# Optimization experiments

Hardware: AMD Instinct MI355X
Metric: run time of the kernel (lower is better)

## Reference

```python
import jax, jax.numpy as jnp
import numpy as np

B, S = 1, 128            # batch, timesteps
N_LGN = 17400            # LGN input units (dense_shape[1])
N_POST = 50000           # V1 neurons (dense_shape[0])
NNZ = 800000             # number of synapses
N_BASIS = 5              # synaptic receptor basis functions
N_RECEPT = 10            # receptor types


def setup_inputs() -> dict:
    key = jax.random.key(0)
    k1, k2, k3, k4, k5, k6 = jax.random.split(key, 6)
    inp = jax.random.normal(k1, (B, S, N_LGN), dtype=jnp.float32)
    rows = jax.random.randint(k2, (NNZ,), 0, N_POST)
    cols = jax.random.randint(k3, (NNZ,), 0, N_LGN)
    indices = jnp.stack([rows, cols], axis=1)  # [nnz, 2] sparse coords
    weights = jax.random.normal(k4, (NNZ,), dtype=jnp.float32)
    synaptic_weights = jax.random.uniform(k5, (N_RECEPT, N_BASIS), dtype=jnp.float32)
    syn_ids = jax.random.randint(k6, (NNZ,), 0, N_RECEPT)
    return {
        "inp": inp,
        "indices": indices,
        "weights": weights,
        "synaptic_weights": synaptic_weights,
        "syn_ids": syn_ids,
        "n_neurons": N_POST,
    }


def reference(inp, indices, weights, synaptic_weights, syn_ids, n_neurons):
    b, s, n_lgn = inp.shape
    x = inp.reshape(b * s, n_lgn)               # [Bt, n_lgn], Bt = batch*time
    rows = indices[:, 0]                        # post-synaptic neuron id
    cols = indices[:, 1]                        # pre-synaptic LGN id
    factors = synaptic_weights[syn_ids]         # [nnz, n_basis] (tf.gather)
    xg = x.T[cols]                              # [nnz, Bt] gathered presyn activity
    n_basis = factors.shape[1]
    outs = []
    for r in range(n_basis):                    # small fixed loop over receptor bases
        vals = weights * factors[:, r]          # per-receptor sparse values
        # sparse_dense_matmul(sparse_w_in, inp, adjoint_b=True) == scatter-add over rows
        outs.append(jax.ops.segment_sum(xg * vals[:, None], rows, num_segments=n_neurons))
    i_in = jnp.stack(outs)                      # [n_basis, n_post, Bt]
    out = jnp.transpose(i_in, (2, 1, 0))        # [Bt, n_post, n_basis]
    return out.reshape(b, s, -1)                # [batch, time, n_post*n_basis]
```

## Files before the change

### kernel.cpp

```cpp
#include <hip/hip_runtime.h>
#include <hip/hip_bf16.h>
#include <stdint.h>

#define N_LGN   17400
#define N_POST  50000
#define NNZ     800000
#define N_BASIS 5
#define ELL_CAP 48

#define NBKT      196
#define NBKT_H    391
#define CAPB      5120
#define BIN_CHUNK 4096
#define BIN_BLOCKS ((NNZ + BIN_CHUNK - 1) / BIN_CHUNK)

#define TPOSE_CBLK   32
#define TPOSE_BLOCKS ((N_LGN + TPOSE_CBLK - 1) / TPOSE_CBLK)

__global__ __launch_bounds__(256) void k_prep(const float* __restrict__ inp,
                                              __hip_bfloat162* __restrict__ xTb,
                                              const int2* __restrict__ idx2,
                                              const float* __restrict__ w,
                                              const int* __restrict__ syn,
                                              int* __restrict__ bucketCnt,
                                              int2* __restrict__ bEdges) {
    __shared__ alignas(16) int2 ebuf[BIN_CHUNK];
    __shared__ unsigned char sbuf[BIN_CHUNK];
    __shared__ int hcnt[256], hstart[256], hcur[256], gbase[256];
    int tid = threadIdx.x;
    if (blockIdx.x < BIN_BLOCKS) {
        int base = blockIdx.x * BIN_CHUNK;
        int ne = NNZ - base; if (ne > BIN_CHUNK) ne = BIN_CHUNK;
        hcnt[tid] = 0;
        __syncthreads();
        int2 pk[16]; int bk[16];
#pragma unroll
        for (int i = 0; i < 16; ++i) {
            int p = i * 256 + tid;
            bk[i] = -1;
            if (p < ne) {
                int2 rc = idx2[base + p];
                float wv = w[base + p];
                int sy = syn[base + p];
                int b  = rc.x >> 8;
                int rl = rc.x & 255;
                pk[i] = make_int2(rc.y | (sy << 15) | (rl << 19), __float_as_int(wv));
                bk[i] = b;
                atomicAdd(&hcnt[b], 1);
            }
        }
        __syncthreads();
        int v = hcnt[tid];
        hstart[tid] = v;
        __syncthreads();
        for (int off = 1; off < 256; off <<= 1) {
            int t = (tid >= off) ? hstart[tid - off] : 0;
            __syncthreads();
            hstart[tid] += t;
            __syncthreads();
        }
        int excl = hstart[tid] - v;
        hstart[tid] = excl;
        hcur[tid]  = excl;
        if (tid < NBKT) gbase[tid] = atomicAdd(&bucketCnt[tid], v);
        __syncthreads();
#pragma unroll
        for (int i = 0; i < 16; ++i) {
            if (bk[i] >= 0) {
                int pos = atomicAdd(&hcur[bk[i]], 1);
                ebuf[pos] = pk[i];
                sbuf[pos] = (unsigned char)bk[i];
            }
        }
        __syncthreads();
        for (int p = tid; p < ne; p += 256) {
            int b  = sbuf[p];
            int gi = gbase[b] + (p - hstart[b]);
            if (gi < CAPB) bEdges[b * CAPB + gi] = ebuf[p];
        }
    } else {
        float* tile = (float*)ebuf;
        int c0 = (blockIdx.x - BIN_BLOCKS) * TPOSE_CBLK;
        for (int it = 0; it < 16; ++it) {
            int flat = it * 256 + tid;
            int s  = flat >> 5;
            int cl = flat & 31;
            int c  = c0 + cl;
            float v = 0.0f;
            if (c < N_LGN) v = inp[s * N_LGN + c];
            tile[cl * 129 + s] = v;
        }
        __syncthreads();
        for (int it = 0; it < 8; ++it) {
            int flat = it * 256 + tid;
            int cl = flat >> 6;
            int sp = flat & 63;
            int c  = c0 + cl;
            if (c < N_LGN) {
                float2 f = make_float2(tile[cl * 129 + 2 * sp], tile[cl * 129 + 2 * sp + 1]);
                xTb[c * 64 + sp] = __float22bfloat162_rn(f);
            }
        }
    }
}

__global__ __launch_bounds__(512) void k_build(const int2* __restrict__ bEdges,
                                               const int* __restrict__ bucketCnt,
                                               int2* __restrict__ ell,
                                               int* __restrict__ counts) {
    __shared__ alignas(16) int2 slab[128 * ELL_CAP];
    __shared__ int rcnt[128];
    int tid   = threadIdx.x;
    int hb    = blockIdx.x;
    int B     = hb >> 1;
    int rbase = (hb & 1) << 7;
    if (tid < 128) rcnt[tid] = 0;
    {
        int4* s4w = (int4*)slab;
        for (int i = tid; i < 128 * ELL_CAP / 2; i += 512) s4w[i] = make_int4(0, 0, 0, 0);
    }
    __syncthreads();
    int cnt = bucketCnt[B]; if (cnt > CAPB) cnt = CAPB;
    for (int p = tid; p < cnt; p += 512) {
        int2 e = bEdges[B * CAPB + p];
        int rl = (e.x >> 19) & 0xFF;
        int r2 = rl - rbase;
        if ((unsigned)r2 < 128u) {
            int r = atomicAdd(&rcnt[r2], 1);
            if (r < ELL_CAP)
                slab[r2 * ELL_CAP + r] =
                    make_int2((e.x & 0x7FFF) | (((e.x >> 15) & 0xF) << 16), e.y);
        }
    }
    __syncthreads();
    int row0  = hb << 7;
    int nrows = N_POST - row0; if (nrows > 128) nrows = 128;
    if (nrows <= 0) return;
    const int4* s4 = (const int4*)slab;
    int4* e4 = (int4*)(ell + (size_t)row0 * ELL_CAP);
    int n4 = nrows * ELL_CAP / 2;
    for (int i = tid; i < n4; i += 512) e4[i] = s4[i];
    if (tid < nrows) counts[row0 + tid] = rcnt[tid];
}

__global__ __launch_bounds__(256) void k_transpose_bf16(const float* __restrict__ inp,
                                                        __hip_bfloat162* __restrict__ xTb) {
    __shared__ float tile[64 * 129];
    int c0  = blockIdx.x * 64;
    int tid = threadIdx.x;
    for (int it = 0; it < 32; ++it) {
        int flat = it * 256 + tid;
        int s  = flat >> 6;
        int cl = flat & 63;
        int c  = c0 + cl;
        float v = 0.0f;
        if (c < N_LGN) v = inp[s * N_LGN + c];
        tile[cl * 129 + s] = v;
    }
    __syncthreads();
    for (int it = 0; it < 16; ++it) {
        int flat = it * 256 + tid;
        int cl = flat >> 6;
        int sp = flat & 63;
        int c  = c0 + cl;
        if (c < N_LGN) {
            float2 f = make_float2(tile[cl * 129 + 2 * sp], tile[cl * 129 + 2 * sp + 1]);
            xTb[c * 64 + sp] = __float22bfloat162_rn(f);
        }
    }
}

__global__ __launch_bounds__(256) void k_hist(const int4* __restrict__ idx2,
                                              int* __restrict__ counts) {
    int t = blockIdx.x * 256 + threadIdx.x;
    if (t >= NNZ / 2) return;
    int4 rc = idx2[t];
    atomicAdd(&counts[rc.x], 1);
    atomicAdd(&counts[rc.z], 1);
}

__global__ __launch_bounds__(1024) void k_scan1(const int* __restrict__ counts,
                                                int* __restrict__ rowStart,
                                                int* __restrict__ blockSums) {
    __shared__ int tmp[1024];
    int tid = threadIdx.x;
    int gid = blockIdx.x * 1024 + tid;
    int v = (gid < N_POST) ? counts[gid] : 0;
    tmp[tid] = v;
    __syncthreads();
    for (int off = 1; off < 1024; off <<= 1) {
        int t = (tid >= off) ? tmp[tid - off] : 0;
        __syncthreads();
        tmp[tid] += t;
        __syncthreads();
    }
    if (gid < N_POST) rowStart[gid] = tmp[tid] - v;
    if (tid == 1023) blockSums[blockIdx.x] = tmp[1023];
}

__global__ __launch_bounds__(64) void k_scan2(const int* __restrict__ blockSums,
                                              int* __restrict__ blockOffsets, int nblk) {
    __shared__ int tmp[64];
    int tid = threadIdx.x;
    int v = (tid < nblk) ? blockSums[tid] : 0;
    tmp[tid] = v;
    __syncthreads();
    for (int off = 1; off < 64; off <<= 1) {
        int t = (tid >= off) ? tmp[tid - off] : 0;
        __syncthreads();
        tmp[tid] += t;
        __syncthreads();
    }
    if (tid < nblk) blockOffsets[tid] = tmp[tid] - v;
}

__global__ __launch_bounds__(1024) void k_scan3(int* __restrict__ rowStart,
                                                const int* __restrict__ blockOffsets) {
    int gid = blockIdx.x * 1024 + threadIdx.x;
    if (gid < N_POST) rowStart[gid] += blockOffsets[blockIdx.x];
}

__global__ __launch_bounds__(256) void k_scatter_csr(const int4* __restrict__ idx2,
                                                     const float2* __restrict__ w2,
                                                     const int2* __restrict__ syn2,
                                                     const int* __restrict__ rowStart,
                                                     int* __restrict__ cursor,
                                                     int2* __restrict__ edges) {
    int t = blockIdx.x * 256 + threadIdx.x;
    if (t >= NNZ / 2) return;
    int4 rc = idx2[t];
    float2 ww = w2[t];
    int2 sy = syn2[t];
    int p0 = rowStart[rc.x] + atomicAdd(&cursor[rc.x], 1);
    edges[p0] = make_int2(rc.y | (sy.x << 16), __float_as_int(ww.x));
    int p1 = rowStart[rc.z] + atomicAdd(&cursor[rc.z], 1);
    edges[p1] = make_int2(rc.w | (sy.y << 16), __float_as_int(ww.y));
}

#define EDGE_FMA2(P0, P1, XW, FA, F4)                                             \
    P0[0] = fmaf((XW).x, (FA).x, P0[0]); P1[0] = fmaf((XW).y, (FA).x, P1[0]);     \
    P0[1] = fmaf((XW).x, (FA).y, P0[1]); P1[1] = fmaf((XW).y, (FA).y, P1[1]);     \
    P0[2] = fmaf((XW).x, (FA).z, P0[2]); P1[2] = fmaf((XW).y, (FA).z, P1[2]);     \
    P0[3] = fmaf((XW).x, (FA).w, P0[3]); P1[3] = fmaf((XW).y, (FA).w, P1[3]);     \
    P0[4] = fmaf((XW).x, (F4),   P0[4]); P1[4] = fmaf((XW).y, (F4),   P1[4]);

#define FINISH_STREAM(P0, P1, X, EX, EY)                                          \
    {                                                                             \
        int sy_  = (EX) >> 16;                                                    \
        float w_ = __int_as_float(EY);                                            \
        float4 fA_ = *(const float4*)&facsP[sy_ * 8];                             \
        float  f4_ = facsP[sy_ * 8 + 4];                                          \
        float2 xw_ = make_float2((X).x * w_, (X).y * w_);                         \
        EDGE_FMA2(P0, P1, xw_, fA_, f4_)                                          \
    }

__global__ __launch_bounds__(512, 8) void k_compute_ell(const __hip_bfloat162* __restrict__ xTb,
                                                        const int2* __restrict__ ell,
                                                        const int* __restrict__ counts,
                                                        const float* __restrict__ sw,
                                                        float2* __restrict__ out2) {
    __shared__ alignas(16) float facsP[80];
    __shared__ float accLds[40 * 133];
    __shared__ alignas(16) int2 eLds[16 * ELL_CAP];
    int tid  = threadIdx.x;
    int wave = tid >> 6;
    int lane = tid & 63;
    int n0   = blockIdx.x * 16;

    if (tid < 50) facsP[(tid / 5) * 8 + (tid % 5)] = sw[tid];
    if (tid < 16 * ELL_CAP / 2)
        ((int4*)eLds)[tid] = ((const int4*)(ell + (size_t)n0 * ELL_CAP))[tid];
    int cA = counts[n0 + wave];     if (cA > ELL_CAP) cA = ELL_CAP;
    int cB = counts[n0 + 8 + wave]; if (cB > ELL_CAP) cB = ELL_CAP;
    __syncthreads();

    float aA0[N_BASIS] = {0.f, 0.f, 0.f, 0.f, 0.f};
    float aA1[N_BASIS] = {0.f, 0.f, 0.f, 0.f, 0.f};
    float aB0[N_BASIS] = {0.f, 0.f, 0.f, 0.f, 0.f};
    float aB1[N_BASIS] = {0.f, 0.f, 0.f, 0.f, 0.f};

    const int4* epA = (const int4*)(eLds + wave * ELL_CAP);
    const int4* epB = (const int4*)(eLds + (wave + 8) * ELL_CAP);
    int mc = cA > cB ? cA : cB;
    for (int j = 0; j < mc; j += 2) {
        int h = j >> 1;
        int4 A = epA[h];
        int4 B = epB[h];
        float2 xA0 = __bfloat1622float2(xTb[(A.x & 0xFFFF) * 64 + lane]);
        float2 xA1 = __bfloat1622float2(xTb[(A.z & 0xFFFF) * 64 + lane]);
        float2 xB0 = __bfloat1622float2(xTb[(B.x & 0xFFFF) * 64 + lane]);
        float2 xB1 = __bfloat1622float2(xTb[(B.z & 0xFFFF) * 64 + lane]);
        FINISH_STREAM(aA0, aA1, xA0, A.x, A.y)
        FINISH_STREAM(aA0, aA1, xA1, A.z, A.w)
        FINISH_STREAM(aB0, aB1, xB0, B.x, B.y)
        FINISH_STREAM(aB0, aB1, xB1, B.z, B.w)
    }

    int base2 = blockIdx.x * 40;
#pragma unroll
    for (int r = 0; r < N_BASIS; ++r) {
        int jj = wave * 5 + r;
        accLds[jj * 133 + 2 * lane]     = aA0[r];
        accLds[jj * 133 + 2 * lane + 1] = aA1[r];
    }
    __syncthreads();
    for (int it = 0; it < 5; ++it) {
        int flat = it * 512 + tid;
        int s  = flat / 20;
        int jj = flat % 20;
        float f0 = accLds[(2 * jj) * 133 + s];
        float f1 = accLds[(2 * jj + 1) * 133 + s];
        out2[s * 125000 + base2 + jj] = make_float2(f0, f1);
    }
    __syncthreads();
#pragma unroll
    for (int r = 0; r < N_BASIS; ++r) {
        int jj = wave * 5 + r;
        accLds[jj * 133 + 2 * lane]     = aB0[r];
        accLds[jj * 133 + 2 * lane + 1] = aB1[r];
    }
    __syncthreads();
    for (int it = 0; it < 5; ++it) {
        int flat = it * 512 + tid;
        int s  = flat / 20;
        int jj = flat % 20;
        float f0 = accLds[(2 * jj) * 133 + s];
        float f1 = accLds[(2 * jj + 1) * 133 + s];
        out2[s * 125000 + base2 + 20 + jj] = make_float2(f0, f1);
    }
}

__global__ __launch_bounds__(512, 8) void k_compute(const __hip_bfloat162* __restrict__ xTb,
                                                    const int2* __restrict__ edges,
                                                    const int* __restrict__ rowStart,
                                                    const int* __restrict__ counts,
                                                    const float* __restrict__ sw,
                                                    float2* __restrict__ out2) {
    __shared__ alignas(16) float facsP[80];
    __shared__ float accLds[40 * 133];
    int tid  = threadIdx.x;
    int wave = tid >> 6;
    int lane = tid & 63;
    int n    = blockIdx.x * 8 + wave;
    int cnt  = counts[n];

    if (tid < 50) facsP[(tid / 5) * 8 + (tid % 5)] = sw[tid];
    __syncthreads();

    float a0[N_BASIS] = {0.f, 0.f, 0.f, 0.f, 0.f};
    float a1[N_BASIS] = {0.f, 0.f, 0.f, 0.f, 0.f};

    const int2* ep = edges + rowStart[n];
    int j = 0;
    for (; j + 1 < cnt; j += 2) {
        int2 e0 = ep[j];
        int2 e1 = ep[j + 1];
        float2 x0 = __bfloat1622float2(xTb[(e0.x & 0xFFFF) * 64 + lane]);
        float2 x1 = __bfloat1622float2(xTb[(e1.x & 0xFFFF) * 64 + lane]);
        FINISH_STREAM(a0, a1, x0, e0.x, e0.y)
        FINISH_STREAM(a0, a1, x1, e1.x, e1.y)
    }
    if (j < cnt) {
        int2 e0 = ep[j];
        float2 x0 = __bfloat1622float2(xTb[(e0.x & 0xFFFF) * 64 + lane]);
        FINISH_STREAM(a0, a1, x0, e0.x, e0.y)
    }

#pragma unroll
    for (int r = 0; r < N_BASIS; ++r) {
        int jj = wave * 5 + r;
        accLds[jj * 133 + 2 * lane]     = a0[r];
        accLds[jj * 133 + 2 * lane + 1] = a1[r];
    }
    __syncthreads();

    int base2 = blockIdx.x * 20;
    for (int it = 0; it < 5; ++it) {
        int flat = it * 512 + tid;
        int s  = flat / 20;
        int jj = flat % 20;
        float f0 = accLds[(2 * jj) * 133 + s];
        float f1 = accLds[(2 * jj + 1) * 133 + s];
        out2[s * 125000 + base2 + jj] = make_float2(f0, f1);
    }
}

extern "C" void kernel_launch(void* const* d_in, const int* in_sizes, int n_in,
                              void* d_out, int out_size, void* d_ws, size_t ws_size,
                              hipStream_t stream) {
    const float* inp     = (const float*)d_in[0];
    const int*   indices = (const int*)d_in[1];
    const float* weights = (const float*)d_in[2];
    const float* sw      = (const float*)d_in[3];
    const int*   syn     = (const int*)d_in[4];

    char* ws = (char*)d_ws;
    __hip_bfloat162* xTb = (__hip_bfloat162*)(ws);
    int* counts          = (int*)(ws + 4454400);

    const size_t ELL_BYTES_END = 4654400ULL + (size_t)N_POST * ELL_CAP * 8;
    bool useEll = (ws_size >= ELL_BYTES_END);

    if (useEll) {
        int2* ell = (int2*)(ws + 4654400);
        int2* bEdges   = (int2*)d_out;
        int*  bucketCnt = (int*)((char*)d_out + (size_t)NBKT * CAPB * 8);
        hipMemsetAsync(bucketCnt, 0, 1024, stream);
        k_prep<<<BIN_BLOCKS + TPOSE_BLOCKS, 256, 0, stream>>>(
            inp, xTb, (const int2*)indices, weights, syn, bucketCnt, bEdges);
        k_build<<<NBKT_H, 512, 0, stream>>>(bEdges, bucketCnt, ell, counts);
        k_compute_ell<<<N_POST / 16, 512, 0, stream>>>(xTb, ell, counts, sw,
                                                       (float2*)d_out);
    } else {
        int* cursor    = (int*)(ws + 4654400);
        int* rowStart  = (int*)(ws + 4854400);
        int* blockSums = (int*)(ws + 5054400);
        int* blockOffs = (int*)(ws + 5054656);
        int2* edges    = (int2*)(ws + 5054912);
        hipMemsetAsync(counts, 0, 400000, stream);
        k_transpose_bf16<<<(N_LGN + 63) / 64, 256, 0, stream>>>(inp, xTb);
        k_hist<<<(NNZ / 2 + 255) / 256, 256, 0, stream>>>((const int4*)indices, counts);
        k_scan1<<<(N_POST + 1023) / 1024, 1024, 0, stream>>>(counts, rowStart, blockSums);
        k_scan2<<<1, 64, 0, stream>>>(blockSums, blockOffs, (N_POST + 1023) / 1024);
        k_scan3<<<(N_POST + 1023) / 1024, 1024, 0, stream>>>(rowStart, blockOffs);
        k_scatter_csr<<<(NNZ / 2 + 255) / 256, 256, 0, stream>>>(
            (const int4*)indices, (const float2*)weights, (const int2*)syn,
            rowStart, cursor, edges);
        k_compute<<<N_POST / 8, 512, 0, stream>>>(xTb, edges, rowStart, counts, sw,
                                                  (float2*)d_out);
    }
}
```

Baseline: 203.3 us.

## Split time dimension into two halves across blocks with half-wave edge parallelism

The transposed bf16 input is stored as two separate halves of the time axis, each 32 pairs wide. Each compute block now handles one time half for a group of 16 neurons, and each wave splits into two 32-lane sub-groups that process alternate edges. Partial sums are combined with a cross-lane shuffle before the LDS transpose. This doubles the block count and shrinks the per-edge gather footprint, aiming for better L2 locality of each xT half and more parallelism. In exchange, edge lists are read twice and extra shuffle and tail work is added.

New measurement: 204.7 us. No clear change (+0.7%).

```diff
diff --git a/kernel.cpp b/kernel.cpp
--- a/kernel.cpp
+++ b/kernel.cpp
@@ -16,6 +16,8 @@
 
 #define TPOSE_CBLK   32
 #define TPOSE_BLOCKS ((N_LGN + TPOSE_CBLK - 1) / TPOSE_CBLK)
+
+#define XH_STRIDE (N_LGN * 32)
 
 __global__ __launch_bounds__(256) void k_prep(const float* __restrict__ inp,
                                               __hip_bfloat162* __restrict__ xTb,
@@ -98,7 +100,8 @@
             int c  = c0 + cl;
             if (c < N_LGN) {
                 float2 f = make_float2(tile[cl * 129 + 2 * sp], tile[cl * 129 + 2 * sp + 1]);
-                xTb[c * 64 + sp] = __float22bfloat162_rn(f);
+                int hh = sp >> 5, j = sp & 31;
+                xTb[hh * XH_STRIDE + c * 32 + j] = __float22bfloat162_rn(f);
             }
         }
     }
@@ -260,12 +263,16 @@
                                                         const float* __restrict__ sw,
                                                         float2* __restrict__ out2) {
     __shared__ alignas(16) float facsP[80];
-    __shared__ float accLds[40 * 133];
+    __shared__ float accLds[40 * 67];
     __shared__ alignas(16) int2 eLds[16 * ELL_CAP];
     int tid  = threadIdx.x;
     int wave = tid >> 6;
     int lane = tid & 63;
-    int n0   = blockIdx.x * 16;
+    int m    = blockIdx.x & 7;
+    int h    = m >> 2;
+    int g    = (blockIdx.x >> 3) * 4 + (m & 3);
+    if (g >= N_POST / 16) return;
+    int n0   = g * 16;
 
     if (tid < 50) facsP[(tid / 5) * 8 + (tid % 5)] = sw[tid];
     if (tid < 16 * ELL_CAP / 2)
@@ -279,54 +286,78 @@
     float aB0[N_BASIS] = {0.f, 0.f, 0.f, 0.f, 0.f};
     float aB1[N_BASIS] = {0.f, 0.f, 0.f, 0.f, 0.f};
 
+    const __hip_bfloat162* xh = xTb + h * XH_STRIDE;
     const int4* epA = (const int4*)(eLds + wave * ELL_CAP);
     const int4* epB = (const int4*)(eLds + (wave + 8) * ELL_CAP);
+    int sub = lane >> 5;
+    int j   = lane & 31;
     int mc = cA > cB ? cA : cB;
-    for (int j = 0; j < mc; j += 2) {
-        int h = j >> 1;
-        int4 A = epA[h];
-        int4 B = epB[h];
-        float2 xA0 = __bfloat1622float2(xTb[(A.x & 0xFFFF) * 64 + lane]);
-        float2 xA1 = __bfloat1622float2(xTb[(A.z & 0xFFFF) * 64 + lane]);
-        float2 xB0 = __bfloat1622float2(xTb[(B.x & 0xFFFF) * 64 + lane]);
-        float2 xB1 = __bfloat1622float2(xTb[(B.z & 0xFFFF) * 64 + lane]);
-        FINISH_STREAM(aA0, aA1, xA0, A.x, A.y)
-        FINISH_STREAM(aA0, aA1, xA1, A.z, A.w)
-        FINISH_STREAM(aB0, aB1, xB0, B.x, B.y)
-        FINISH_STREAM(aB0, aB1, xB1, B.z, B.w)
-    }
-
-    int base2 = blockIdx.x * 40;
+    for (int e = 0; e < mc; e += 4) {
+        int hh = e >> 1;
+        int4 A0 = epA[hh], A1 = epA[hh + 1];
+        int4 B0 = epB[hh], B1 = epB[hh + 1];
+        int ea0 = sub ? A0.z : A0.x;  int wa0 = sub ? A0.w : A0.y;
+        int ea1 = sub ? A1.z : A1.x;  int wa1 = sub ? A1.w : A1.y;
+        int eb0 = sub ? B0.z : B0.x;  int wb0 = sub ? B0.w : B0.y;
+        int eb1 = sub ? B1.z : B1.x;  int wb1 = sub ? B1.w : B1.y;
+        float2 xA0 = __bfloat1622float2(xh[(ea0 & 0xFFFF) * 32 + j]);
+        float2 xA1 = __bfloat1622float2(xh[(ea1 & 0xFFFF) * 32 + j]);
+        float2 xB0 = __bfloat1622float2(xh[(eb0 & 0xFFFF) * 32 + j]);
+        float2 xB1 = __bfloat1622float2(xh[(eb1 & 0xFFFF) * 32 + j]);
+        FINISH_STREAM(aA0, aA1, xA0, ea0, wa0)
+        FINISH_STREAM(aA0, aA1, xA1, ea1, wa1)
+        FINISH_STREAM(aB0, aB1, xB0, eb0, wb0)
+        FINISH_STREAM(aB0, aB1, xB1, eb1, wb1)
+    }
+
 #pragma unroll
     for (int r = 0; r < N_BASIS; ++r) {
-        int jj = wave * 5 + r;
-        accLds[jj * 133 + 2 * lane]     = aA0[r];
-        accLds[jj * 133 + 2 * lane + 1] = aA1[r];
-    }
-    __syncthreads();
-    for (int it = 0; it < 5; ++it) {
+        aA0[r] += __shfl_xor(aA0[r], 32);
+        aA1[r] += __shfl_xor(aA1[r], 32);
+        aB0[r] += __shfl_xor(aB0[r], 32);
+        aB1[r] += __shfl_xor(aB1[r], 32);
+    }
+
+    int base2 = g * 40;
+    int sbase = h * 64;
+    if (lane < 32) {
+#pragma unroll
+        for (int r = 0; r < N_BASIS; ++r) {
+            int jj = wave * 5 + r;
+            accLds[jj * 67 + 2 * lane]     = aA0[r];
+            accLds[jj * 67 + 2 * lane + 1] = aA1[r];
+        }
+    }
+    __syncthreads();
+    for (int it = 0; it < 3; ++it) {
         int flat = it * 512 + tid;
-        int s  = flat / 20;
-        int jj = flat % 20;
-        float f0 = accLds[(2 * jj) * 133 + s];
-        float f1 = accLds[(2 * jj + 1) * 133 + s];
-        out2[s * 125000 + base2 + jj] = make_float2(f0, f1);
-    }
-    __syncthreads();
-#pragma unroll
-    for (int r = 0; r < N_BASIS; ++r) {
-        int jj = wave * 5 + r;
-        accLds[jj * 133 + 2 * lane]     = aB0[r];
-        accLds[jj * 133 + 2 * lane + 1] = aB1[r];
-    }
-    __syncthreads();
-    for (int it = 0; it < 5; ++it) {
+        if (flat < 1280) {
+            int s  = flat / 20;
+            int jj = flat % 20;
+            float f0 = accLds[(2 * jj) * 67 + s];
+            float f1 = accLds[(2 * jj + 1) * 67 + s];
+            out2[(sbase + s) * 125000 + base2 + jj] = make_float2(f0, f1);
+        }
+    }
+    __syncthreads();
+    if (lane < 32) {
+#pragma unroll
+        for (int r = 0; r < N_BASIS; ++r) {
+            int jj = wave * 5 + r;
+            accLds[jj * 67 + 2 * lane]     = aB0[r];
+            accLds[jj * 67 + 2 * lane + 1] = aB1[r];
+        }
+    }
+    __syncthreads();
+    for (int it = 0; it < 3; ++it) {
         int flat = it * 512 + tid;
-        int s  = flat / 20;
-        int jj = flat % 20;
-        float f0 = accLds[(2 * jj) * 133 + s];
-        float f1 = accLds[(2 * jj + 1) * 133 + s];
-        out2[s * 125000 + base2 + 20 + jj] = make_float2(f0, f1);
+        if (flat < 1280) {
+            int s  = flat / 20;
+            int jj = flat % 20;
+            float f0 = accLds[(2 * jj) * 67 + s];
+            float f1 = accLds[(2 * jj + 1) * 67 + s];
+            out2[(sbase + s) * 125000 + base2 + 20 + jj] = make_float2(f0, f1);
+        }
     }
 }
 
@@ -409,8 +440,8 @@
         k_prep<<<BIN_BLOCKS + TPOSE_BLOCKS, 256, 0, stream>>>(
             inp, xTb, (const int2*)indices, weights, syn, bucketCnt, bEdges);
         k_build<<<NBKT_H, 512, 0, stream>>>(bEdges, bucketCnt, ell, counts);
-        k_compute_ell<<<N_POST / 16, 512, 0, stream>>>(xTb, ell, counts, sw,
-                                                       (float2*)d_out);
+        k_compute_ell<<<(N_POST / 16 + 3) / 4 * 8, 512, 0, stream>>>(
+            xTb, ell, counts, sw, (float2*)d_out);
     } else {
         int* cursor    = (int*)(ws + 4654400);
         int* rowStart  = (int*)(ws + 4854400);
```
